# Kernel optimization log

Hardware: AMD Instinct MI355X
Metric: run time of the kernel (lower is better)

## Reference

```python
import jax, jax.numpy as jnp
import numpy as np

T_CH = 512
C_CH = 512
RED = 16
K = int(T_CH * 0.3)  # 153


def setup_inputs() -> dict:
    key = jax.random.key(0)
    ks = jax.random.split(key, 12)
    h_t, h_c = T_CH // RED, C_CH // RED
    s = 0.05
    return {
        "x_t": jax.random.normal(ks[0], (16, T_CH, 64, 64), jnp.float32),
        "x_c": jax.random.normal(ks[1], (16, C_CH, 64, 64), jnp.float32),
        # SE branch t: Linear(T,T/r) -> ReLU -> Linear(T/r,T) -> Sigmoid (weights stored as (in,out))
        "w1_t": jax.random.normal(ks[2], (T_CH, h_t), jnp.float32) * s,
        "b1_t": jnp.zeros((h_t,), jnp.float32),
        "w2_t": jax.random.normal(ks[3], (h_t, T_CH), jnp.float32) * s,
        "b2_t": jnp.zeros((T_CH,), jnp.float32),
        # SE branch c
        "w1_c": jax.random.normal(ks[4], (C_CH, h_c), jnp.float32) * s,
        "b1_c": jnp.zeros((h_c,), jnp.float32),
        "w2_c": jax.random.normal(ks[5], (h_c, C_CH), jnp.float32) * s,
        "b2_c": jnp.zeros((C_CH,), jnp.float32),
        # cross-channel attention parameter, shape (t_channels, c_channels)
        "cross_att": jax.random.normal(ks[6], (T_CH, C_CH), jnp.float32),
    }


def reference(x_t, x_c, w1_t, b1_t, w2_t, b2_t, w1_c, b1_c, w2_c, b2_c, cross_att):
    ct = x_t.shape[1]
    # AdaptiveAvgPool2d(1) -> global mean over spatial, then SE MLP + sigmoid
    att_t = jnp.mean(x_t, axis=(2, 3))                      # [b, ct]
    att_t = jax.nn.sigmoid(jax.nn.relu(att_t @ w1_t + b1_t) @ w2_t + b2_t)
    att_c = jnp.mean(x_c, axis=(2, 3))                      # [b, cc]
    att_c = jax.nn.sigmoid(jax.nn.relu(att_c @ w1_c + b1_c) @ w2_c + b2_c)

    # top-k hard mask over t-channels (scatter of constant 1.0)
    _, topk_idx = jax.lax.top_k(att_t, K)                   # [b, K]
    sparse_att_t = jax.nn.one_hot(topk_idx, ct, dtype=att_t.dtype).sum(axis=1)  # [b, ct]

    cross_w = jax.nn.softmax(cross_att, axis=-1)            # [ct, cc]

    # einsum('bt,tc,bchw->bthw'): GEMM over channels then broadcast mask
    cross_t = sparse_att_t[:, :, None, None] * jnp.einsum('tc,bchw->bthw', cross_w, x_c)
    # einsum('bc,tc,bthw->bchw') with cross_w.T labeled 'tc' => sum_t cross_w[c,t] * x_t
    cross_c = att_c[:, :, None, None] * jnp.einsum('ct,bthw->bchw', cross_w, x_t)

    out_t = x_t * att_t[:, :, None, None] + cross_t
    out_c = x_c * att_c[:, :, None, None] + cross_c
    return out_t, out_c
```

## Files before the change

kernel.cpp:

```cpp
#include <hip/hip_runtime.h>

#define NBATCH 16
#define CH 512
#define HID 32
#define KTOP 153
#define SP 4096
#define NELEM (NBATCH*CH*SP)

typedef __bf16 bf16x8 __attribute__((ext_vector_type(8)));
typedef float f32x16 __attribute__((ext_vector_type(16)));

__device__ __forceinline__ unsigned short f2bf(float f) {
    union { float f; unsigned u; } v; v.f = f;
    unsigned r = v.u + 0x7FFFu + ((v.u >> 16) & 1u);
    return (unsigned short)(r >> 16);
}

__global__ __launch_bounds__(256) void k1_reduce(
    const float* __restrict__ xt, const float* __restrict__ xc,
    float* __restrict__ psum)
{
    int c4 = blockIdx.x, bz = blockIdx.y;
    int b = bz >> 1, br = bz & 1;
    const float* x = br ? xc : xt;
    int t = threadIdx.x, lane = t & 63, w = t >> 6;
    int ch = c4 * 4 + w;
    const float4* p = (const float4*)(x + ((size_t)b * CH + ch) * SP);
    float s = 0.f;
    #pragma unroll
    for (int k = 0; k < 16; ++k) {
        float4 v = p[lane + k * 64];
        s += ((v.x + v.y) + (v.z + v.w));
    }
    #pragma unroll
    for (int off = 32; off; off >>= 1) s += __shfl_xor(s, off, 64);
    if (lane == 0) psum[(size_t)(br * 16 + b) * CH + ch] = s;
}

__global__ __launch_bounds__(512) void k2_se(
    const float* __restrict__ psum,
    const float* __restrict__ w1t, const float* __restrict__ b1t,
    const float* __restrict__ w2t, const float* __restrict__ b2t,
    const float* __restrict__ w1c, const float* __restrict__ b1c,
    const float* __restrict__ w2c, const float* __restrict__ b2c,
    float* __restrict__ sAt, float* __restrict__ sBt, float* __restrict__ attc)
{
    int b = blockIdx.x, br = blockIdx.y;
    int bb = br * 16 + b;
    int t = threadIdx.x;
    __shared__ float satt[512];
    __shared__ float ph[16][33];
    __shared__ float sh[32];
    __shared__ float sval[512];

    satt[t] = psum[(size_t)bb * CH + t] * (1.0f / 4096.0f);
    __syncthreads();

    const float* w1 = br ? w1c : w1t; const float* b1 = br ? b1c : b1t;
    const float* w2 = br ? w2c : w2t; const float* b2 = br ? b2c : b2t;

    {
        int j = t & 31, seg = t >> 5;
        float hp = 0.f;
        #pragma unroll
        for (int i = 0; i < 32; ++i)
            hp += satt[seg * 32 + i] * w1[(seg * 32 + i) * HID + j];
        ph[seg][j] = hp;
    }
    __syncthreads();
    if (t < HID) {
        float h = b1[t];
        #pragma unroll
        for (int sgi = 0; sgi < 16; ++sgi) h += ph[sgi][t];
        sh[t] = fmaxf(h, 0.0f);
    }
    __syncthreads();

    float z = b2[t];
    #pragma unroll
    for (int j = 0; j < HID; ++j) z += sh[j] * w2[j * CH + t];
    float a = 1.0f / (1.0f + expf(-z));

    if (br == 0) {
        sval[t] = a;
        __syncthreads();
        int cnt = 0;
        for (int j = 0; j < CH; ++j) {
            float o = sval[j];
            cnt += (o > a) || (o == a && j < t);
        }
        sAt[b * CH + t] = a;
        sBt[b * CH + t] = (cnt < KTOP) ? 1.0f : 0.0f;
    } else {
        attc[b * CH + t] = a;
    }
}

__global__ __launch_bounds__(64) void k2_softmax(
    const float* __restrict__ ca, unsigned short* __restrict__ wswz)
{
    int trow = blockIdx.x;
    int lane = threadIdx.x;
    const float* row = ca + (size_t)trow * CH;
    float v[8];
    #pragma unroll
    for (int i = 0; i < 8; ++i) v[i] = row[lane * 8 + i];
    float m = v[0];
    #pragma unroll
    for (int i = 1; i < 8; ++i) m = fmaxf(m, v[i]);
    #pragma unroll
    for (int off = 32; off; off >>= 1) m = fmaxf(m, __shfl_xor(m, off, 64));
    float s = 0.f;
    #pragma unroll
    for (int i = 0; i < 8; ++i) { v[i] = expf(v[i] - m); s += v[i]; }
    #pragma unroll
    for (int off = 32; off; off >>= 1) s += __shfl_xor(s, off, 64);
    float inv = 1.0f / s;

    int k = lane * 8;
    int kb = k >> 5, ks = (k >> 4) & 1, hi = (k >> 3) & 1;
    int p = ((kb * 16 + (trow >> 5)) * 2 + ks) * 64 + hi * 32 + (trow & 31);
    unsigned short* dst = wswz + (size_t)p * 8;
    ushort4 lo, hm;
    lo.x = f2bf(v[0] * inv); lo.y = f2bf(v[1] * inv);
    lo.z = f2bf(v[2] * inv); lo.w = f2bf(v[3] * inv);
    hm.x = f2bf(v[4] * inv); hm.y = f2bf(v[5] * inv);
    hm.z = f2bf(v[6] * inv); hm.w = f2bf(v[7] * inv);
    *(ushort4*)dst = lo;
    *(ushort4*)(dst + 4) = hm;
}

__global__ __launch_bounds__(256, 2) void k3_fused(
    const float* __restrict__ xt, const float* __restrict__ xc,
    const unsigned short* __restrict__ wswz,
    const float* __restrict__ sAt, const float* __restrict__ sBt,
    const float* __restrict__ attc,
    float* __restrict__ out)
{
    int nt = blockIdx.x, b = blockIdx.y;
    int t = threadIdx.x, lane = t & 63, w = t >> 6;
    int n0 = nt * 32;

    __shared__ unsigned short B2[2][32 * 512];

    {
        int a  = t & 7;
        int cq = t >> 3;
        #pragma unroll
        for (int src = 0; src < 2; ++src) {
            const float* x = src ? xc : xt;
            char* bl = (char*)B2[src];
            const float* gbase = x + (size_t)b * CH * SP + n0 + a * 4;
            #pragma unroll
            for (int chb = 0; chb < 4; ++chb) {
                int q = chb * 32 + cq;
                float4 v0 = *(const float4*)(gbase + (size_t)(q * 4 + 0) * SP);
                float4 v1 = *(const float4*)(gbase + (size_t)(q * 4 + 1) * SP);
                float4 v2 = *(const float4*)(gbase + (size_t)(q * 4 + 2) * SP);
                float4 v3 = *(const float4*)(gbase + (size_t)(q * 4 + 3) * SP);
                #pragma unroll
                for (int j = 0; j < 4; ++j) {
                    int n = a * 4 + j;
                    ushort4 d;
                    d.x = f2bf(((const float*)&v0)[j]);
                    d.y = f2bf(((const float*)&v1)[j]);
                    d.z = f2bf(((const float*)&v2)[j]);
                    d.w = f2bf(((const float*)&v3)[j]);
                    int bo = n * 1024 + ((q * 8) ^ ((n & 7) << 4));
                    *(ushort4*)(bl + bo) = d;
                }
            }
        }
    }
    __syncthreads();

    f32x16 acct[4], accc[4];
    #pragma unroll
    for (int r = 0; r < 4; ++r)
        #pragma unroll
        for (int e = 0; e < 16; ++e) { acct[r][e] = 0.0f; accc[r][e] = 0.0f; }

    const unsigned short* abase = wswz + ((size_t)(w * 4 * 2 * 64 + lane)) * 8;
    const char* btl = (const char*)B2[0];
    const char* bcl = (const char*)B2[1];
    int nb = (lane & 31) * 1024;
    int xr = (lane & 7) << 4;
    int kf = (lane >> 5) * 16;

    bf16x8 afr[2][8], bft[2][2], bfc[2][2];

    #pragma unroll
    for (int r = 0; r < 4; ++r)
        #pragma unroll
        for (int ks = 0; ks < 2; ++ks)
            afr[0][r * 2 + ks] = *(const bf16x8*)(abase + r * 1024 + ks * 512);
    #pragma unroll
    for (int ks = 0; ks < 2; ++ks) {
        int off = nb + ((ks * 32 + kf) ^ xr);
        bft[0][ks] = *(const bf16x8*)(btl + off);
        bfc[0][ks] = *(const bf16x8*)(bcl + off);
    }

    #pragma unroll
    for (int kb = 0; kb < 16; ++kb) {
        int cur = kb & 1, nxt = cur ^ 1;
        if (kb < 15) {
            #pragma unroll
            for (int r = 0; r < 4; ++r)
                #pragma unroll
                for (int ks = 0; ks < 2; ++ks)
                    afr[nxt][r * 2 + ks] =
                        *(const bf16x8*)(abase + (kb + 1) * 16384 + r * 1024 + ks * 512);
            #pragma unroll
            for (int ks = 0; ks < 2; ++ks) {
                int off = nb + ((((kb + 1) * 64) + ks * 32 + kf) ^ xr);
                bft[nxt][ks] = *(const bf16x8*)(btl + off);
                bfc[nxt][ks] = *(const bf16x8*)(bcl + off);
            }
        }
        #pragma unroll
        for (int ks = 0; ks < 2; ++ks)
            #pragma unroll
            for (int r = 0; r < 4; ++r) {
                acct[r] = __builtin_amdgcn_mfma_f32_32x32x16_bf16(
                    afr[cur][r * 2 + ks], bfc[cur][ks], acct[r], 0, 0, 0);
                accc[r] = __builtin_amdgcn_mfma_f32_32x32x16_bf16(
                    afr[cur][r * 2 + ks], bft[cur][ks], accc[r], 0, 0, 0);
            }
    }

    int colb = n0 + (lane & 31);
    int rowq = 4 * (lane >> 5);
    #pragma unroll
    for (int r = 0; r < 4; ++r) {
        #pragma unroll
        for (int reg = 0; reg < 16; ++reg) {
            int m = w * 128 + r * 32 + (reg & 3) + 8 * (reg >> 2) + rowq;
            size_t idx = ((size_t)b * CH + m) * SP + colb;
            float at = sAt[b * CH + m];
            float bt = sBt[b * CH + m];
            float ac = attc[b * CH + m];
            float ot = at * xt[idx] + bt * acct[r][reg];
            float oc = ac * xc[idx] + ac * accc[r][reg];
            __builtin_nontemporal_store(ot, &out[idx]);
            __builtin_nontemporal_store(oc, &out[NELEM + idx]);
        }
    }
}

extern "C" void kernel_launch(void* const* d_in, const int* in_sizes, int n_in,
                              void* d_out, int out_size, void* d_ws, size_t ws_size,
                              hipStream_t stream)
{
    const float* xt  = (const float*)d_in[0];
    const float* xc  = (const float*)d_in[1];
    const float* w1t = (const float*)d_in[2];
    const float* b1t = (const float*)d_in[3];
    const float* w2t = (const float*)d_in[4];
    const float* b2t = (const float*)d_in[5];
    const float* w1c = (const float*)d_in[6];
    const float* b1c = (const float*)d_in[7];
    const float* w2c = (const float*)d_in[8];
    const float* b2c = (const float*)d_in[9];
    const float* ca  = (const float*)d_in[10];
    float* out = (float*)d_out;
    char* ws = (char*)d_ws;

    unsigned short* wswz = (unsigned short*)(ws);
    float* psum = (float*)(ws + 524288ull);
    float* sAt  = (float*)(ws + 589824ull);
    float* sBt  = (float*)(ws + 622592ull);
    float* attc = (float*)(ws + 655360ull);

    hipLaunchKernelGGL(k1_reduce, dim3(128, 32), dim3(256), 0, stream,
                       xt, xc, psum);
    hipLaunchKernelGGL(k2_se, dim3(16, 2), dim3(512), 0, stream,
                       psum, w1t, b1t, w2t, b2t, w1c, b1c, w2c, b2c, sAt, sBt, attc);
    hipLaunchKernelGGL(k2_softmax, dim3(512), dim3(64), 0, stream, ca, wswz);
    hipLaunchKernelGGL(k3_fused, dim3(128, 16), dim3(256), 0, stream,
                       xt, xc, wswz, sAt, sBt, attc, out);
}
```

Baseline: 671.5 us.

## Make fused GEMM kernel persistent with double-buffered LDS staging of input tiles

```diff
diff --git a/kernel.cpp b/kernel.cpp
--- a/kernel.cpp
+++ b/kernel.cpp
@@ -130,121 +130,156 @@
     *(ushort4*)(dst + 4) = hm;
 }
 
-__global__ __launch_bounds__(256, 2) void k3_fused(
+__global__ __launch_bounds__(512, 2) void k3_fused(
     const float* __restrict__ xt, const float* __restrict__ xc,
     const unsigned short* __restrict__ wswz,
     const float* __restrict__ sAt, const float* __restrict__ sBt,
     const float* __restrict__ attc,
     float* __restrict__ out)
 {
-    int nt = blockIdx.x, b = blockIdx.y;
+    int blk = blockIdx.x;
+    int b = blk >> 4, tg = blk & 15;
     int t = threadIdx.x, lane = t & 63, w = t >> 6;
-    int n0 = nt * 32;
-
-    __shared__ unsigned short B2[2][32 * 512];
+
+    __shared__ unsigned short B2[2][2][32 * 512];
+
+    int a  = t & 7;
+    int sc = (t >> 3) & 1;
+    int cq = t >> 4;
+    const float* xsrc = sc ? xc : xt;
+    const float* gstage = xsrc + (size_t)b * CH * SP + tg * 256 + a * 4;
+
+    const unsigned short* abase = wswz + (size_t)(w * 2) * 1024 + lane * 8;
+    int nb = (lane & 31) * 1024;
+    int xr = (lane & 7) << 4;
+    int kf = (lane >> 5) * 16;
 
     {
-        int a  = t & 7;
-        int cq = t >> 3;
-        #pragma unroll
-        for (int src = 0; src < 2; ++src) {
-            const float* x = src ? xc : xt;
-            char* bl = (char*)B2[src];
-            const float* gbase = x + (size_t)b * CH * SP + n0 + a * 4;
+        float4 sv[16];
+        #pragma unroll
+        for (int chb = 0; chb < 4; ++chb)
+            #pragma unroll
+            for (int r2 = 0; r2 < 4; ++r2) {
+                int ch = (chb * 32 + cq) * 4 + r2;
+                sv[chb * 4 + r2] = *(const float4*)(gstage + (size_t)ch * SP);
+            }
+        char* bl = (char*)B2[0][sc];
+        #pragma unroll
+        for (int chb = 0; chb < 4; ++chb) {
+            int q = chb * 32 + cq;
+            #pragma unroll
+            for (int j = 0; j < 4; ++j) {
+                int n = a * 4 + j;
+                ushort4 d;
+                d.x = f2bf(((const float*)&sv[chb * 4 + 0])[j]);
+                d.y = f2bf(((const float*)&sv[chb * 4 + 1])[j]);
+                d.z = f2bf(((const float*)&sv[chb * 4 + 2])[j]);
+                d.w = f2bf(((const float*)&sv[chb * 4 + 3])[j]);
+                *(ushort4*)(bl + n * 1024 + ((q * 8) ^ ((n & 7) << 4))) = d;
+            }
+        }
+    }
+    __syncthreads();
+
+    #pragma unroll 1
+    for (int i = 0; i < 8; ++i) {
+        int buf = i & 1;
+        int n0 = tg * 256 + i * 32;
+
+        float4 sv[16];
+        if (i < 7) {
+            const float* g = gstage + (i + 1) * 32;
+            #pragma unroll
+            for (int chb = 0; chb < 4; ++chb)
+                #pragma unroll
+                for (int r2 = 0; r2 < 4; ++r2) {
+                    int ch = (chb * 32 + cq) * 4 + r2;
+                    sv[chb * 4 + r2] = *(const float4*)(g + (size_t)ch * SP);
+                }
+        }
+        __builtin_amdgcn_sched_barrier(0);
+
+        f32x16 acct[2], accc[2];
+        #pragma unroll
+        for (int r = 0; r < 2; ++r)
+            #pragma unroll
+            for (int e = 0; e < 16; ++e) { acct[r][e] = 0.0f; accc[r][e] = 0.0f; }
+
+        const char* btl = (const char*)B2[buf][0];
+        const char* bcl = (const char*)B2[buf][1];
+
+        bf16x8 afr[2][4];
+        #pragma unroll
+        for (int r = 0; r < 2; ++r)
+            #pragma unroll
+            for (int ks = 0; ks < 2; ++ks)
+                afr[0][r * 2 + ks] = *(const bf16x8*)(abase + r * 1024 + ks * 512);
+
+        #pragma unroll
+        for (int kb = 0; kb < 16; ++kb) {
+            int cur = kb & 1, nxt = cur ^ 1;
+            if (kb < 15) {
+                #pragma unroll
+                for (int r = 0; r < 2; ++r)
+                    #pragma unroll
+                    for (int ks = 0; ks < 2; ++ks)
+                        afr[nxt][r * 2 + ks] =
+                            *(const bf16x8*)(abase + (kb + 1) * 16384 + r * 1024 + ks * 512);
+            }
+            bf16x8 bft[2], bfc[2];
+            #pragma unroll
+            for (int ks = 0; ks < 2; ++ks) {
+                int off = nb + ((kb * 64 + ks * 32 + kf) ^ xr);
+                bft[ks] = *(const bf16x8*)(btl + off);
+                bfc[ks] = *(const bf16x8*)(bcl + off);
+            }
+            #pragma unroll
+            for (int ks = 0; ks < 2; ++ks)
+                #pragma unroll
+                for (int r = 0; r < 2; ++r) {
+                    acct[r] = __builtin_amdgcn_mfma_f32_32x32x16_bf16(
+                        afr[cur][r * 2 + ks], bfc[ks], acct[r], 0, 0, 0);
+                    accc[r] = __builtin_amdgcn_mfma_f32_32x32x16_bf16(
+                        afr[cur][r * 2 + ks], bft[ks], accc[r], 0, 0, 0);
+                }
+        }
+
+        if (i < 7) {
+            char* bl = (char*)B2[buf ^ 1][sc];
             #pragma unroll
             for (int chb = 0; chb < 4; ++chb) {
                 int q = chb * 32 + cq;
-                float4 v0 = *(const float4*)(gbase + (size_t)(q * 4 + 0) * SP);
-                float4 v1 = *(const float4*)(gbase + (size_t)(q * 4 + 1) * SP);
-                float4 v2 = *(const float4*)(gbase + (size_t)(q * 4 + 2) * SP);
-                float4 v3 = *(const float4*)(gbase + (size_t)(q * 4 + 3) * SP);
                 #pragma unroll
                 for (int j = 0; j < 4; ++j) {
                     int n = a * 4 + j;
                     ushort4 d;
-                    d.x = f2bf(((const float*)&v0)[j]);
-                    d.y = f2bf(((const float*)&v1)[j]);
-                    d.z = f2bf(((const float*)&v2)[j]);
-                    d.w = f2bf(((const float*)&v3)[j]);
-                    int bo = n * 1024 + ((q * 8) ^ ((n & 7) << 4));
-                    *(ushort4*)(bl + bo) = d;
+                    d.x = f2bf(((const float*)&sv[chb * 4 + 0])[j]);
+                    d.y = f2bf(((const float*)&sv[chb * 4 + 1])[j]);
+                    d.z = f2bf(((const float*)&sv[chb * 4 + 2])[j]);
+                    d.w = f2bf(((const float*)&sv[chb * 4 + 3])[j]);
+                    *(ushort4*)(bl + n * 1024 + ((q * 8) ^ ((n & 7) << 4))) = d;
                 }
             }
         }
-    }
-    __syncthreads();
-
-    f32x16 acct[4], accc[4];
-    #pragma unroll
-    for (int r = 0; r < 4; ++r)
-        #pragma unroll
-        for (int e = 0; e < 16; ++e) { acct[r][e] = 0.0f; accc[r][e] = 0.0f; }
-
-    const unsigned short* abase = wswz + ((size_t)(w * 4 * 2 * 64 + lane)) * 8;
-    const char* btl = (const char*)B2[0];
-    const char* bcl = (const char*)B2[1];
-    int nb = (lane & 31) * 1024;
-    int xr = (lane & 7) << 4;
-    int kf = (lane >> 5) * 16;
-
-    bf16x8 afr[2][8], bft[2][2], bfc[2][2];
-
-    #pragma unroll
-    for (int r = 0; r < 4; ++r)
-        #pragma unroll
-        for (int ks = 0; ks < 2; ++ks)
-            afr[0][r * 2 + ks] = *(const bf16x8*)(abase + r * 1024 + ks * 512);
-    #pragma unroll
-    for (int ks = 0; ks < 2; ++ks) {
-        int off = nb + ((ks * 32 + kf) ^ xr);
-        bft[0][ks] = *(const bf16x8*)(btl + off);
-        bfc[0][ks] = *(const bf16x8*)(bcl + off);
-    }
-
-    #pragma unroll
-    for (int kb = 0; kb < 16; ++kb) {
-        int cur = kb & 1, nxt = cur ^ 1;
-        if (kb < 15) {
-            #pragma unroll
-            for (int r = 0; r < 4; ++r)
-                #pragma unroll
-                for (int ks = 0; ks < 2; ++ks)
-                    afr[nxt][r * 2 + ks] =
-                        *(const bf16x8*)(abase + (kb + 1) * 16384 + r * 1024 + ks * 512);
-            #pragma unroll
-            for (int ks = 0; ks < 2; ++ks) {
-                int off = nb + ((((kb + 1) * 64) + ks * 32 + kf) ^ xr);
-                bft[nxt][ks] = *(const bf16x8*)(btl + off);
-                bfc[nxt][ks] = *(const bf16x8*)(bcl + off);
-            }
-        }
-        #pragma unroll
-        for (int ks = 0; ks < 2; ++ks)
-            #pragma unroll
-            for (int r = 0; r < 4; ++r) {
-                acct[r] = __builtin_amdgcn_mfma_f32_32x32x16_bf16(
-                    afr[cur][r * 2 + ks], bfc[cur][ks], acct[r], 0, 0, 0);
-                accc[r] = __builtin_amdgcn_mfma_f32_32x32x16_bf16(
-                    afr[cur][r * 2 + ks], bft[cur][ks], accc[r], 0, 0, 0);
-            }
-    }
-
-    int colb = n0 + (lane & 31);
-    int rowq = 4 * (lane >> 5);
-    #pragma unroll
-    for (int r = 0; r < 4; ++r) {
-        #pragma unroll
-        for (int reg = 0; reg < 16; ++reg) {
-            int m = w * 128 + r * 32 + (reg & 3) + 8 * (reg >> 2) + rowq;
-            size_t idx = ((size_t)b * CH + m) * SP + colb;
-            float at = sAt[b * CH + m];
-            float bt = sBt[b * CH + m];
-            float ac = attc[b * CH + m];
-            float ot = at * xt[idx] + bt * acct[r][reg];
-            float oc = ac * xc[idx] + ac * accc[r][reg];
-            __builtin_nontemporal_store(ot, &out[idx]);
-            __builtin_nontemporal_store(oc, &out[NELEM + idx]);
-        }
+
+        int colb = n0 + (lane & 31);
+        int rowq = 4 * (lane >> 5);
+        #pragma unroll
+        for (int r = 0; r < 2; ++r) {
+            #pragma unroll
+            for (int reg = 0; reg < 16; ++reg) {
+                int m = w * 64 + r * 32 + (reg & 3) + 8 * (reg >> 2) + rowq;
+                size_t idx = ((size_t)b * CH + m) * SP + colb;
+                float at = sAt[b * CH + m];
+                float bt = sBt[b * CH + m];
+                float ac = attc[b * CH + m];
+                float ot = at * xt[idx] + bt * acct[r][reg];
+                float oc = ac * xc[idx] + ac * accc[r][reg];
+                __builtin_nontemporal_store(ot, &out[idx]);
+                __builtin_nontemporal_store(oc, &out[NELEM + idx]);
+            }
+        }
+        __syncthreads();
     }
 }
 
@@ -277,6 +312,6 @@
     hipLaunchKernelGGL(k2_se, dim3(16, 2), dim3(512), 0, stream,
                        psum, w1t, b1t, w2t, b2t, w1c, b1c, w2c, b2c, sAt, sBt, attc);
     hipLaunchKernelGGL(k2_softmax, dim3(512), dim3(64), 0, stream, ca, wswz);
-    hipLaunchKernelGGL(k3_fused, dim3(128, 16), dim3(256), 0, stream,
+    hipLaunchKernelGGL(k3_fused, dim3(256), dim3(512), 0, stream,
                        xt, xc, wswz, sAt, sBt, attc, out);
 }
```

Result: slower. 1.157 ms (+72.4%).

## Split fused GEMM block into two row-halves with eight waves per block

Applied to the files above, without the earlier changes.

```diff
diff --git a/kernel.cpp b/kernel.cpp
--- a/kernel.cpp
+++ b/kernel.cpp
@@ -130,14 +130,17 @@
     *(ushort4*)(dst + 4) = hm;
 }
 
-__global__ __launch_bounds__(256, 2) void k3_fused(
+__global__ __launch_bounds__(512, 4) void k3_fused(
     const float* __restrict__ xt, const float* __restrict__ xc,
     const unsigned short* __restrict__ wswz,
     const float* __restrict__ sAt, const float* __restrict__ sBt,
     const float* __restrict__ attc,
     float* __restrict__ out)
 {
-    int nt = blockIdx.x, b = blockIdx.y;
+    int id = blockIdx.x;
+    int lane8 = id & 7, half = (id >> 3) & 1, pslot = id >> 4;
+    int tile = pslot * 8 + lane8;
+    int b = tile >> 7, nt = tile & 127;
     int t = threadIdx.x, lane = t & 63, w = t >> 6;
     int n0 = nt * 32;
 
@@ -145,106 +148,88 @@
 
     {
         int a  = t & 7;
-        int cq = t >> 3;
-        #pragma unroll
-        for (int src = 0; src < 2; ++src) {
-            const float* x = src ? xc : xt;
-            char* bl = (char*)B2[src];
-            const float* gbase = x + (size_t)b * CH * SP + n0 + a * 4;
+        int sc = (t >> 3) & 1;
+        int cq = t >> 4;
+        const float* xsrc = sc ? xc : xt;
+        const float* gbase = xsrc + (size_t)b * CH * SP + n0 + a * 4;
+        char* bl = (char*)B2[sc];
+        #pragma unroll
+        for (int chb = 0; chb < 4; ++chb) {
+            int q = chb * 32 + cq;
+            float4 v0 = *(const float4*)(gbase + (size_t)(q * 4 + 0) * SP);
+            float4 v1 = *(const float4*)(gbase + (size_t)(q * 4 + 1) * SP);
+            float4 v2 = *(const float4*)(gbase + (size_t)(q * 4 + 2) * SP);
+            float4 v3 = *(const float4*)(gbase + (size_t)(q * 4 + 3) * SP);
             #pragma unroll
-            for (int chb = 0; chb < 4; ++chb) {
-                int q = chb * 32 + cq;
-                float4 v0 = *(const float4*)(gbase + (size_t)(q * 4 + 0) * SP);
-                float4 v1 = *(const float4*)(gbase + (size_t)(q * 4 + 1) * SP);
-                float4 v2 = *(const float4*)(gbase + (size_t)(q * 4 + 2) * SP);
-                float4 v3 = *(const float4*)(gbase + (size_t)(q * 4 + 3) * SP);
-                #pragma unroll
-                for (int j = 0; j < 4; ++j) {
-                    int n = a * 4 + j;
-                    ushort4 d;
-                    d.x = f2bf(((const float*)&v0)[j]);
-                    d.y = f2bf(((const float*)&v1)[j]);
-                    d.z = f2bf(((const float*)&v2)[j]);
-                    d.w = f2bf(((const float*)&v3)[j]);
-                    int bo = n * 1024 + ((q * 8) ^ ((n & 7) << 4));
-                    *(ushort4*)(bl + bo) = d;
-                }
+            for (int j = 0; j < 4; ++j) {
+                int n = a * 4 + j;
+                ushort4 d;
+                d.x = f2bf(((const float*)&v0)[j]);
+                d.y = f2bf(((const float*)&v1)[j]);
+                d.z = f2bf(((const float*)&v2)[j]);
+                d.w = f2bf(((const float*)&v3)[j]);
+                *(ushort4*)(bl + n * 1024 + ((q * 8) ^ ((n & 7) << 4))) = d;
             }
         }
     }
     __syncthreads();
 
-    f32x16 acct[4], accc[4];
-    #pragma unroll
-    for (int r = 0; r < 4; ++r)
-        #pragma unroll
-        for (int e = 0; e < 16; ++e) { acct[r][e] = 0.0f; accc[r][e] = 0.0f; }
-
-    const unsigned short* abase = wswz + ((size_t)(w * 4 * 2 * 64 + lane)) * 8;
+    int mb = half * 8 + w;
+
+    f32x16 acct, accc;
+    #pragma unroll
+    for (int e = 0; e < 16; ++e) { acct[e] = 0.0f; accc[e] = 0.0f; }
+
+    const unsigned short* abase = wswz + mb * 1024 + (size_t)lane * 8;
     const char* btl = (const char*)B2[0];
     const char* bcl = (const char*)B2[1];
     int nb = (lane & 31) * 1024;
     int xr = (lane & 7) << 4;
     int kf = (lane >> 5) * 16;
 
-    bf16x8 afr[2][8], bft[2][2], bfc[2][2];
-
-    #pragma unroll
-    for (int r = 0; r < 4; ++r)
-        #pragma unroll
-        for (int ks = 0; ks < 2; ++ks)
-            afr[0][r * 2 + ks] = *(const bf16x8*)(abase + r * 1024 + ks * 512);
-    #pragma unroll
-    for (int ks = 0; ks < 2; ++ks) {
-        int off = nb + ((ks * 32 + kf) ^ xr);
-        bft[0][ks] = *(const bf16x8*)(btl + off);
-        bfc[0][ks] = *(const bf16x8*)(bcl + off);
-    }
+    bf16x8 afr[2][2];
+    #pragma unroll
+    for (int ks = 0; ks < 2; ++ks)
+        afr[0][ks] = *(const bf16x8*)(abase + ks * 512);
 
     #pragma unroll
     for (int kb = 0; kb < 16; ++kb) {
         int cur = kb & 1, nxt = cur ^ 1;
         if (kb < 15) {
             #pragma unroll
-            for (int r = 0; r < 4; ++r)
-                #pragma unroll
-                for (int ks = 0; ks < 2; ++ks)
-                    afr[nxt][r * 2 + ks] =
-                        *(const bf16x8*)(abase + (kb + 1) * 16384 + r * 1024 + ks * 512);
-            #pragma unroll
-            for (int ks = 0; ks < 2; ++ks) {
-                int off = nb + ((((kb + 1) * 64) + ks * 32 + kf) ^ xr);
-                bft[nxt][ks] = *(const bf16x8*)(btl + off);
-                bfc[nxt][ks] = *(const bf16x8*)(bcl + off);
-            }
-        }
-        #pragma unroll
-        for (int ks = 0; ks < 2; ++ks)
-            #pragma unroll
-            for (int r = 0; r < 4; ++r) {
-                acct[r] = __builtin_amdgcn_mfma_f32_32x32x16_bf16(
-                    afr[cur][r * 2 + ks], bfc[cur][ks], acct[r], 0, 0, 0);
-                accc[r] = __builtin_amdgcn_mfma_f32_32x32x16_bf16(
-                    afr[cur][r * 2 + ks], bft[cur][ks], accc[r], 0, 0, 0);
-            }
+            for (int ks = 0; ks < 2; ++ks)
+                afr[nxt][ks] = *(const bf16x8*)(abase + (kb + 1) * 16384 + ks * 512);
+        }
+        bf16x8 bft[2], bfc[2];
+        #pragma unroll
+        for (int ks = 0; ks < 2; ++ks) {
+            int off = nb + ((kb * 64 + ks * 32 + kf) ^ xr);
+            bft[ks] = *(const bf16x8*)(btl + off);
+            bfc[ks] = *(const bf16x8*)(bcl + off);
+        }
+        #pragma unroll
+        for (int ks = 0; ks < 2; ++ks) {
+            acct = __builtin_amdgcn_mfma_f32_32x32x16_bf16(
+                afr[cur][ks], bfc[ks], acct, 0, 0, 0);
+            accc = __builtin_amdgcn_mfma_f32_32x32x16_bf16(
+                afr[cur][ks], bft[ks], accc, 0, 0, 0);
+        }
     }
 
     int colb = n0 + (lane & 31);
     int rowq = 4 * (lane >> 5);
-    #pragma unroll
-    for (int r = 0; r < 4; ++r) {
-        #pragma unroll
-        for (int reg = 0; reg < 16; ++reg) {
-            int m = w * 128 + r * 32 + (reg & 3) + 8 * (reg >> 2) + rowq;
-            size_t idx = ((size_t)b * CH + m) * SP + colb;
-            float at = sAt[b * CH + m];
-            float bt = sBt[b * CH + m];
-            float ac = attc[b * CH + m];
-            float ot = at * xt[idx] + bt * acct[r][reg];
-            float oc = ac * xc[idx] + ac * accc[r][reg];
-            __builtin_nontemporal_store(ot, &out[idx]);
-            __builtin_nontemporal_store(oc, &out[NELEM + idx]);
-        }
+    int mbase = mb * 32;
+    #pragma unroll
+    for (int reg = 0; reg < 16; ++reg) {
+        int m = mbase + (reg & 3) + 8 * (reg >> 2) + rowq;
+        size_t idx = ((size_t)b * CH + m) * SP + colb;
+        float at = sAt[b * CH + m];
+        float bt = sBt[b * CH + m];
+        float ac = attc[b * CH + m];
+        float ot = at * xt[idx] + bt * acct[reg];
+        float oc = ac * (xc[idx] + accc[reg]);
+        __builtin_nontemporal_store(ot, &out[idx]);
+        __builtin_nontemporal_store(oc, &out[NELEM + idx]);
     }
 }
 
@@ -277,6 +262,6 @@
     hipLaunchKernelGGL(k2_se, dim3(16, 2), dim3(512), 0, stream,
                        psum, w1t, b1t, w2t, b2t, w1c, b1c, w2c, b2c, sAt, sBt, attc);
     hipLaunchKernelGGL(k2_softmax, dim3(512), dim3(64), 0, stream, ca, wswz);
-    hipLaunchKernelGGL(k3_fused, dim3(128, 16), dim3(256), 0, stream,
+    hipLaunchKernelGGL(k3_fused, dim3(4096), dim3(512), 0, stream,
                        xt, xc, wswz, sAt, sBt, attc, out);
 }
```

Measured after the change: 580.6 us. 13.5% less time.
